# Kernel tuning notes

Measured on AMD Instinct MI355X. Metric: run time of the kernel, lower is better.

Reference implementation:

```python
import jax, jax.numpy as jnp
import numpy as np

N, E, D, G, OUT, K = 150000, 1200000, 128, 512, 2, 2
EPS = 1e-5


def setup_inputs() -> dict:
    key = jax.random.key(0)
    ks = jax.random.split(key, 8)
    nfeat = jax.random.normal(ks[0], (N, D), dtype=jnp.float32)
    src = jax.random.randint(ks[1], (E,), 0, N, dtype=jnp.int32)
    dst = jax.random.randint(ks[2], (E,), 0, N, dtype=jnp.int32)
    node2graph = jnp.sort(jax.random.randint(ks[3], (N,), 0, G, dtype=jnp.int32))
    s = 1.0 / np.sqrt(D)
    conv_w = jax.random.normal(ks[4], (D, D), dtype=jnp.float32) * s
    conv_b = jnp.zeros((D,), jnp.float32)
    gamma1 = jnp.ones((D,), jnp.float32)
    beta1 = jnp.zeros((D,), jnp.float32)
    gamma2 = jnp.ones((D,), jnp.float32)
    beta2 = jnp.zeros((D,), jnp.float32)
    pred_w = jax.random.normal(ks[5], (D, OUT), dtype=jnp.float32) * s
    pred_b = jnp.zeros((OUT,), jnp.float32)
    return {"nfeat": nfeat, "src": src, "dst": dst, "node2graph": node2graph,
            "num_graphs": G,
            "conv_w": conv_w, "conv_b": conv_b,
            "gamma1": gamma1, "beta1": beta1,
            "gamma2": gamma2, "beta2": beta2,
            "pred_w": pred_w, "pred_b": pred_b}


def _batchnorm(h, gamma, beta):
    # batch-norm over the node dimension (training-mode stats)
    mu = jnp.mean(h, axis=0)
    var = jnp.mean(jnp.square(h - mu), axis=0)
    return (h - mu) * jax.lax.rsqrt(var + EPS) * gamma + beta


def reference(nfeat, src, dst, node2graph, num_graphs,
              conv_w, conv_b, gamma1, beta1, gamma2, beta2, pred_w, pred_b):
    n = nfeat.shape[0]
    # symmetric degree normalization D^{-1/2} A D^{-1/2}
    deg = jax.ops.segment_sum(jnp.ones_like(dst, dtype=nfeat.dtype), dst, num_segments=n)
    dnorm = jax.lax.rsqrt(jnp.clip(deg, 1.0, None))  # [N]
    h = nfeat  # dropout with p=0 is identity
    for _ in range(K):  # k-hop SGC propagation interleaved with norm
        m = (h * dnorm[:, None])[src]                       # [E, D] gather
        h = jax.ops.segment_sum(m, dst, num_segments=n)     # scatter-add
        h = h * dnorm[:, None]
        h = _batchnorm(h, gamma1, beta1)
    h = h @ conv_w + conv_b          # SGConv linear
    h = _batchnorm(h, gamma2, beta2)  # middle norm
    h = jax.nn.relu(h)                # activation (dropout p=0)
    # mean pooling per graph
    cnt = jax.ops.segment_sum(jnp.ones((n,), h.dtype), node2graph, num_segments=num_graphs)
    g = jax.ops.segment_sum(h, node2graph, num_segments=num_graphs)
    g = g / jnp.clip(cnt, 1.0, None)[:, None]
    return g @ pred_w + pred_b  # [G, OUT]
```

## Files before the change

kernel.cpp:

```cpp
#include <hip/hip_runtime.h>
#include <hip/hip_fp16.h>
#include <cstddef>
#include <cstdint>

constexpr int DIMS = 128;
constexpr float BN_EPS = 1e-5f;
constexpr int NSH = 64;
constexpr int GB = 2048;
constexpr int NPB = 512;

typedef _Float16 f16x8 __attribute__((ext_vector_type(8)));
typedef float f32x4 __attribute__((ext_vector_type(4)));

static __device__ __forceinline__ f16x8 as_f16x8(uint4 u) {
  union { uint4 u; f16x8 h; } x; x.u = u; return x.h;
}
static __device__ __forceinline__ __half2 as_h2(uint32_t u) {
  union { uint32_t u; __half2 h; } x; x.u = u; return x.h;
}

__global__ void zero_k(float* __restrict__ fp, size_t nf) {
  size_t i = (size_t)blockIdx.x * blockDim.x + threadIdx.x;
  if (i < nf) fp[i] = 0.f;
}

__global__ void cvt_k(const float* __restrict__ in, uint32_t* __restrict__ out,
                      const int* __restrict__ deg, float* __restrict__ dnorm, size_t n64) {
  size_t i = (size_t)blockIdx.x * blockDim.x + threadIdx.x;
  size_t stride = (size_t)gridDim.x * blockDim.x;
  const float2* in2 = (const float2*)in;
  for (; i < n64; i += stride) {
    size_t row = i >> 6;
    float d = rsqrtf(fmaxf((float)deg[row], 1.0f));
    if ((i & 63) == 0) dnorm[row] = d;
    float2 v = in2[i];
    __half2 h = __floats2half2_rn(v.x * d, v.y * d);
    out[i] = *(const uint32_t*)&h;
  }
}


__global__ __launch_bounds__(256) void cnt_k(const int* __restrict__ dst,
                                             int* __restrict__ C, int e, int chunk) {
  __shared__ int hist[512];
  int b = blockIdx.x;
  for (int j = threadIdx.x; j < 512; j += 256) hist[j] = 0;
  __syncthreads();
  int i0 = b * chunk;
  int i1 = i0 + chunk; if (i1 > e) i1 = e;
  for (int i = i0 + threadIdx.x; i < i1; i += 256)
    atomicAdd(&hist[dst[i] >> 9], 1);
  __syncthreads();
  for (int j = threadIdx.x; j < 512; j += 256) C[b * 512 + j] = hist[j];
}

__global__ __launch_bounds__(512) void colscan_k(int* __restrict__ C, int* __restrict__ tot) {
  int j = blockIdx.x;
  int t = threadIdx.x;
  int v = C[t * 512 + j];
  __shared__ int lds[512];
  lds[t] = v; __syncthreads();
  for (int off = 1; off < 512; off <<= 1) {
    int add = (t >= off) ? lds[t - off] : 0;
    __syncthreads();
    lds[t] += add;
    __syncthreads();
  }
  C[t * 512 + j] = lds[t] - v;
  if (t == 511) tot[j] = lds[511];
}

__global__ __launch_bounds__(512) void bscan_k(const int* __restrict__ tot, int nbins,
                                               int* __restrict__ boff, int e) {
  int t = threadIdx.x;
  int v = tot[t];
  __shared__ int lds[512];
  lds[t] = v; __syncthreads();
  for (int off = 1; off < 512; off <<= 1) {
    int add = (t >= off) ? lds[t - off] : 0;
    __syncthreads();
    lds[t] += add;
    __syncthreads();
  }
  boff[t] = lds[t] - v;
  if (t == 0) boff[nbins] = e;
}

__global__ __launch_bounds__(256) void scat_k(const int* __restrict__ src,
                                              const int* __restrict__ dst,
                                              const int* __restrict__ C,
                                              const int* __restrict__ boff,
                                              int* __restrict__ ebin, int e, int chunk) {
  __shared__ int cur[512];
  int b = blockIdx.x;
  for (int j = threadIdx.x; j < 512; j += 256) cur[j] = boff[j] + C[b * 512 + j];
  __syncthreads();
  int i0 = b * chunk;
  int i1 = i0 + chunk; if (i1 > e) i1 = e;
  for (int i = i0 + threadIdx.x; i < i1; i += 256) {
    int d = dst[i];
    int bin = d >> 9;
    int p = atomicAdd(&cur[bin], 1);
    ebin[p] = (src[i] << 9) | (d & 511);
  }
}

__global__ void deg_bins_k(const int* __restrict__ ebin, const int* __restrict__ boff,
                           int* __restrict__ deg, int n) {
  __shared__ int cnt[512];
  int b = blockIdx.x;
  for (int j = threadIdx.x; j < 512; j += 256) cnt[j] = 0;
  __syncthreads();
  int j0 = boff[b], j1 = boff[b + 1];
  for (int i = j0 + threadIdx.x; i < j1; i += 256) atomicAdd(&cnt[ebin[i] & 511], 1);
  __syncthreads();
  int base = b << 9;
  for (int j = threadIdx.x; j < 512; j += 256) {
    int node = base + j;
    if (node < n) deg[node] = cnt[j];
  }
}

__global__ void scan1_k(const int* __restrict__ deg, int* __restrict__ bsum, int n) {
  __shared__ int lds[256];
  int t = threadIdx.x;
  int base = blockIdx.x * 1024;
  int s = 0;
  for (int i = t; i < 1024; i += 256) {
    int idx = base + i;
    s += (idx < n) ? deg[idx] : 0;
  }
  lds[t] = s; __syncthreads();
  for (int off = 128; off > 0; off >>= 1) {
    if (t < off) lds[t] += lds[t + off];
    __syncthreads();
  }
  if (t == 0) bsum[blockIdx.x] = lds[0];
}

__global__ void scan2_k(int* __restrict__ bsum, int nb, int* __restrict__ row_off, int n, int e) {
  __shared__ int lds[256];
  int t = threadIdx.x;
  int v = (t < nb) ? bsum[t] : 0;
  lds[t] = v; __syncthreads();
  for (int off = 1; off < 256; off <<= 1) {
    int add = (t >= off) ? lds[t - off] : 0;
    __syncthreads();
    lds[t] += add;
    __syncthreads();
  }
  if (t < nb) bsum[t] = lds[t] - v;
  if (t == 0) row_off[n] = e;
}

__global__ void scan3_k(const int* __restrict__ deg, const int* __restrict__ bsum,
                        int* __restrict__ row_off, int n) {
  __shared__ int lds[256];
  int t = threadIdx.x;
  int base = blockIdx.x * 1024 + t * 4;
  int e0 = (base + 0 < n) ? deg[base + 0] : 0;
  int e1 = (base + 1 < n) ? deg[base + 1] : 0;
  int e2 = (base + 2 < n) ? deg[base + 2] : 0;
  int e3 = (base + 3 < n) ? deg[base + 3] : 0;
  int ts = e0 + e1 + e2 + e3;
  lds[t] = ts; __syncthreads();
  for (int off = 1; off < 256; off <<= 1) {
    int add = (t >= off) ? lds[t - off] : 0;
    __syncthreads();
    lds[t] += add;
    __syncthreads();
  }
  int ex = lds[t] - ts + bsum[blockIdx.x];
  if (base + 0 < n) row_off[base + 0] = ex;
  ex += e0;
  if (base + 1 < n) row_off[base + 1] = ex;
  ex += e1;
  if (base + 2 < n) row_off[base + 2] = ex;
  ex += e2;
  if (base + 3 < n) row_off[base + 3] = ex;
}

__global__ __launch_bounds__(512) void adj_bins_k(
    const int* __restrict__ ebin, const int* __restrict__ boff,
    const int* __restrict__ row_off, const float* __restrict__ dnorm,
    int* __restrict__ adj, float* __restrict__ wsum, int n) {
  __shared__ int cur[512];
  __shared__ int ro[512];
  __shared__ float ws[512];
  int b = blockIdx.x;
  int base = b << 9;
  for (int j = threadIdx.x; j < 512; j += 512) {
    cur[j] = 0;
    ws[j] = 0.f;
    int node = base + j;
    ro[j] = (node < n) ? row_off[node] : 0;
  }
  __syncthreads();
  int j0 = boff[b], j1 = boff[b + 1];
  for (int i = j0 + threadIdx.x; i < j1; i += 512) {
    int pk = ebin[i];
    int dl = pk & 511;
    int s = pk >> 9;
    int p = atomicAdd(&cur[dl], 1);
    adj[ro[dl] + p] = s;
    atomicAdd(&ws[dl], dnorm[s]);
  }
  __syncthreads();
  for (int j = threadIdx.x; j < 512; j += 512) {
    int node = base + j;
    if (node < n) wsum[node] = ws[j];
  }
}

template <bool AFF>
__global__ __launch_bounds__(256) void gather_k(
    const uint32_t* __restrict__ Xu, uint32_t* __restrict__ Yout,
    const int* __restrict__ row_off, const int* __restrict__ adj,
    const float* __restrict__ dn, const float* __restrict__ wsum,
    const float* __restrict__ a, const float* __restrict__ b,
    float* __restrict__ sumS, float* __restrict__ sqS, int n, int nwaves) {
  int tid = threadIdx.x;
  int l = tid & 63, w = tid >> 6;
  int wid = blockIdx.x * 4 + w;
  uint32_t lu = (uint32_t)l;
  int f0 = 2 * l;
  float af0 = 1.f, bf0 = 0.f, af1 = 1.f, bf1 = 0.f;
  if (AFF) { af0 = a[f0]; bf0 = b[f0]; af1 = a[f0 + 1]; bf1 = b[f0 + 1]; }
  float s0 = 0.f, s1 = 0.f, q0 = 0.f, q1 = 0.f;

  for (int nodeA = wid; nodeA < n; nodeA += 2 * nwaves) {
    const int nodeB = nodeA + nwaves;
    const bool hasB = nodeB < n;
    int ja = row_off[nodeA];
    const int ea = row_off[nodeA + 1];
    int jb = hasB ? row_off[nodeB] : 0;
    const int eb = hasB ? row_off[nodeB + 1] : 0;
    float accA0 = 0.f, accA1 = 0.f, accB0 = 0.f, accB1 = 0.f;

    while ((ja < ea) || (jb < eb)) {
      uint32_t xa[8], xb[8];
      const bool runA = ja < ea, runB = jb < eb;
      if (runA) {
#pragma unroll
        for (int t = 0; t < 8; ++t) {
          int jj = ja + t;
          int jc = jj < ea ? jj : ea - 1;
          uint32_t sj = (uint32_t)adj[jc];
          uint32_t v = Xu[(sj << 6) + lu];
          xa[t] = (jj < ea) ? v : 0u;
        }
      }
      if (runB) {
#pragma unroll
        for (int t = 0; t < 8; ++t) {
          int jj = jb + t;
          int jc = jj < eb ? jj : eb - 1;
          uint32_t sj = (uint32_t)adj[jc];
          uint32_t v = Xu[(sj << 6) + lu];
          xb[t] = (jj < eb) ? v : 0u;
        }
      }
      if (runA) {
        __half2 t0 = __hadd2(as_h2(xa[0]), as_h2(xa[1]));
        __half2 t1 = __hadd2(as_h2(xa[2]), as_h2(xa[3]));
        __half2 t2 = __hadd2(as_h2(xa[4]), as_h2(xa[5]));
        __half2 t3 = __hadd2(as_h2(xa[6]), as_h2(xa[7]));
        float2 u0 = __half22float2(__hadd2(t0, t1));
        float2 u1 = __half22float2(__hadd2(t2, t3));
        accA0 += u0.x + u1.x;
        accA1 += u0.y + u1.y;
        ja += 8;
      }
      if (runB) {
        __half2 t0 = __hadd2(as_h2(xb[0]), as_h2(xb[1]));
        __half2 t1 = __hadd2(as_h2(xb[2]), as_h2(xb[3]));
        __half2 t2 = __hadd2(as_h2(xb[4]), as_h2(xb[5]));
        __half2 t3 = __hadd2(as_h2(xb[6]), as_h2(xb[7]));
        float2 u0 = __half22float2(__hadd2(t0, t1));
        float2 u1 = __half22float2(__hadd2(t2, t3));
        accB0 += u0.x + u1.x;
        accB1 += u0.y + u1.y;
        jb += 8;
      }
    }

    {
      float dnn = dn[nodeA];
      float v0, v1;
      if constexpr (AFF) {
        float wsn = wsum[nodeA];
        v0 = dnn * fmaf(af0, accA0, bf0 * wsn);
        v1 = dnn * fmaf(af1, accA1, bf1 * wsn);
        __half2 hv = __floats2half2_rn(v0, v1);
        Yout[((uint32_t)nodeA << 6) + lu] = *(const uint32_t*)&hv;
      } else {
        v0 = dnn * accA0;
        v1 = dnn * accA1;
        __half2 hv = __floats2half2_rn(v0 * dnn, v1 * dnn);
        Yout[((uint32_t)nodeA << 6) + lu] = *(const uint32_t*)&hv;
      }
      s0 += v0; s1 += v1; q0 += v0 * v0; q1 += v1 * v1;
    }
    if (hasB) {
      float dnn = dn[nodeB];
      float v0, v1;
      if constexpr (AFF) {
        float wsn = wsum[nodeB];
        v0 = dnn * fmaf(af0, accB0, bf0 * wsn);
        v1 = dnn * fmaf(af1, accB1, bf1 * wsn);
        __half2 hv = __floats2half2_rn(v0, v1);
        Yout[((uint32_t)nodeB << 6) + lu] = *(const uint32_t*)&hv;
      } else {
        v0 = dnn * accB0;
        v1 = dnn * accB1;
        __half2 hv = __floats2half2_rn(v0 * dnn, v1 * dnn);
        Yout[((uint32_t)nodeB << 6) + lu] = *(const uint32_t*)&hv;
      }
      s0 += v0; s1 += v1; q0 += v0 * v0; q1 += v1 * v1;
    }
  }

  __shared__ float red[4][256];
  red[w][l] = s0; red[w][64 + l] = s1; red[w][128 + l] = q0; red[w][192 + l] = q1;
  __syncthreads();
  float t = red[0][tid] + red[1][tid] + red[2][tid] + red[3][tid];
  int comp = tid >> 6, li = tid & 63;
  int sh = blockIdx.x & (NSH - 1);
  float* dstp = ((comp & 2) ? sqS : sumS) + sh * DIMS;
  atomicAdd(&dstp[2 * li + (comp & 1)], t);
}

__global__ void affine_k(const float* __restrict__ sum, const float* __restrict__ sq,
                         const float* __restrict__ gamma, const float* __restrict__ beta,
                         float* __restrict__ a, float* __restrict__ b, float invn) {
  int d = threadIdx.x;
  float s = 0.f, q = 0.f;
  for (int k = 0; k < NSH; ++k) { s += sum[k * DIMS + d]; q += sq[k * DIMS + d]; }
  float mu = s * invn;
  float var = q * invn - mu * mu;
  float rs = rsqrtf(var + BN_EPS);
  float ad = rs * gamma[d];
  a[d] = ad;
  b[d] = beta[d] - mu * ad;
}

__global__ void foldw_k(const float* __restrict__ W, const float* __restrict__ cb,
                        const float* __restrict__ a2, const float* __restrict__ b2,
                        __half* __restrict__ Wt, float* __restrict__ cp) {
  int o = blockIdx.x;
  int d = threadIdx.x;
  float w = W[d * DIMS + o];
  Wt[o * DIMS + d] = __float2half(a2[d] * w);
  __shared__ float red[128];
  red[d] = b2[d] * w;
  __syncthreads();
  for (int off = 64; off > 0; off >>= 1) {
    if (d < off) red[d] += red[d + off];
    __syncthreads();
  }
  if (d == 0) cp[o] = red[0] + cb[o];
}

__global__ __launch_bounds__(256) void matmul_k(
    const uint4* __restrict__ X, const uint4* __restrict__ Wt,
    const float* __restrict__ cp, __half* __restrict__ Z,
    float* __restrict__ sumS, float* __restrict__ sqS, int n) {
  int tid = threadIdx.x;
  int l = tid & 63, w = tid >> 6;
  int rowg = l & 15;
  int kg = l >> 4;
  int r0 = (blockIdx.x * 4 + w) * 16;
  bool active = r0 < n;

  __shared__ float sred[4][128], qred[4][128];
  float svals[8], qvals[8];

  if (active) {
    f32x4 acc[8] = {};
    const uint4* xrow = X + (size_t)(r0 + rowg) * 16;
    bool arow_ok = (r0 + rowg) < n;
#pragma unroll
    for (int kk = 0; kk < 4; ++kk) {
      uint4 au = arow_ok ? xrow[kk * 4 + kg] : make_uint4(0u, 0u, 0u, 0u);
      f16x8 afr = as_f16x8(au);
#pragma unroll
      for (int c = 0; c < 8; ++c) {
        f16x8 bfr = as_f16x8(Wt[(size_t)(c * 16 + rowg) * 16 + kk * 4 + kg]);
        acc[c] = __builtin_amdgcn_mfma_f32_16x16x32_f16(afr, bfr, acc[c], 0, 0, 0);
      }
    }
#pragma unroll
    for (int c = 0; c < 8; ++c) {
      float cpv = cp[c * 16 + rowg];
      float s = 0.f, q = 0.f;
#pragma unroll
      for (int r = 0; r < 4; ++r) {
        int row = r0 + kg * 4 + r;
        float vv = acc[c][r] + cpv;
        bool ok = row < n;
        vv = ok ? vv : 0.f;
        s += vv; q += vv * vv;
        if (ok) Z[(size_t)row * DIMS + c * 16 + rowg] = __float2half(vv);
      }
      s += __shfl_xor(s, 16); s += __shfl_xor(s, 32);
      q += __shfl_xor(q, 16); q += __shfl_xor(q, 32);
      svals[c] = s; qvals[c] = q;
    }
  }
  if (active) {
    if (kg == 0) {
#pragma unroll
      for (int c = 0; c < 8; ++c) {
        sred[w][c * 16 + rowg] = svals[c];
        qred[w][c * 16 + rowg] = qvals[c];
      }
    }
  } else {
    sred[w][l] = 0.f; sred[w][64 + l] = 0.f;
    qred[w][l] = 0.f; qred[w][64 + l] = 0.f;
  }
  __syncthreads();
  int f = tid & 127;
  int sh = blockIdx.x & (NSH - 1);
  if (tid < 128) {
    float s = sred[0][f] + sred[1][f] + sred[2][f] + sred[3][f];
    atomicAdd(&sumS[sh * DIMS + f], s);
  } else {
    float q = qred[0][f] + qred[1][f] + qred[2][f] + qred[3][f];
    atomicAdd(&sqS[sh * DIMS + f], q);
  }
}

__global__ void gstart_k(const int* __restrict__ n2g, int* __restrict__ gstart, int n, int G) {
  int i = blockIdx.x * blockDim.x + threadIdx.x;
  if (i >= n) return;
  int g = n2g[i];
  int gp = (i == 0) ? -1 : n2g[i - 1];
  for (int x = gp + 1; x <= g; ++x) gstart[x] = i;
  if (i == n - 1) {
    for (int x = g + 1; x <= G; ++x) gstart[x] = n;
  }
}

__global__ __launch_bounds__(512) void pool_pred_k(
    const uint4* __restrict__ Z, const int* __restrict__ gstart,
    const float* __restrict__ a3, const float* __restrict__ b3,
    const float* __restrict__ pw, const float* __restrict__ pb,
    float* __restrict__ out) {
  int g = blockIdx.x;
  int tid = threadIdx.x;
  int l = tid & 63, w = tid >> 6;
  int grp = l >> 4, fl = l & 15;
  int f0 = fl * 8;
  float av[8], bv[8];
#pragma unroll
  for (int q = 0; q < 8; ++q) { av[q] = a3[f0 + q]; bv[q] = b3[f0 + q]; }
  int s = gstart[g], e = gstart[g + 1];
  float rs[8] = {0.f, 0.f, 0.f, 0.f, 0.f, 0.f, 0.f, 0.f};
  for (int ni = s + (w * 4 + grp); ni < e; ni += 32) {
    uint4 zv = Z[(size_t)ni * 16 + fl];
    const __half2* h = (const __half2*)&zv;
#pragma unroll
    for (int q = 0; q < 4; ++q) {
      float2 z = __half22float2(h[q]);
      rs[2 * q] += fmaxf(fmaf(z.x, av[2 * q], bv[2 * q]), 0.f);
      rs[2 * q + 1] += fmaxf(fmaf(z.y, av[2 * q + 1], bv[2 * q + 1]), 0.f);
    }
  }
  float p0 = 0.f, p1 = 0.f;
#pragma unroll
  for (int q = 0; q < 8; ++q) {
    p0 += rs[q] * pw[(f0 + q) * 2 + 0];
    p1 += rs[q] * pw[(f0 + q) * 2 + 1];
  }
  __shared__ float r[2][512];
  r[0][tid] = p0; r[1][tid] = p1;
  __syncthreads();
  for (int off = 256; off > 0; off >>= 1) {
    if (tid < off) { r[0][tid] += r[0][tid + off]; r[1][tid] += r[1][tid + off]; }
    __syncthreads();
  }
  if (tid == 0) {
    float inv = 1.f / fmaxf((float)(e - s), 1.f);
    out[g * 2 + 0] = r[0][0] * inv + pb[0];
    out[g * 2 + 1] = r[1][0] * inv + pb[1];
  }
}

extern "C" void kernel_launch(void* const* d_in, const int* in_sizes, int n_in,
                              void* d_out, int out_size, void* d_ws, size_t ws_size,
                              hipStream_t stream) {
  const float* nfeat  = (const float*)d_in[0];
  const int*   src    = (const int*)d_in[1];
  const int*   dst    = (const int*)d_in[2];
  const int*   n2g    = (const int*)d_in[3];
  const float* conv_w = (const float*)d_in[5];
  const float* conv_b = (const float*)d_in[6];
  const float* gamma1 = (const float*)d_in[7];
  const float* beta1  = (const float*)d_in[8];
  const float* gamma2 = (const float*)d_in[9];
  const float* beta2  = (const float*)d_in[10];
  const float* pred_w = (const float*)d_in[11];
  const float* pred_b = (const float*)d_in[12];
  float* out = (float*)d_out;
  (void)n_in; (void)ws_size;

  const int n = in_sizes[0] / DIMS;
  const int e = in_sizes[1];
  const int g = out_size / 2;
  const int nbins = (n + 511) >> 9;

  char* p = (char*)d_ws;
  auto alloc = [&](size_t bytes) { char* r = p; p += (bytes + 255) & ~(size_t)255; return r; };
  uint32_t* Xp  = (uint32_t*)alloc((size_t)n * 64 * 4);
  uint32_t* W1  = (uint32_t*)alloc((size_t)n * 64 * 4);
  uint32_t* Y2  = (uint32_t*)alloc((size_t)n * 64 * 4);
  __half*   Zh  = (__half*)alloc((size_t)n * 64 * 4);
  float* dnorm = (float*)alloc((size_t)n * 4);
  float* stat  = (float*)alloc(((size_t)6 * NSH * DIMS + n) * 4);
  float* wsum  = stat + 6 * NSH * DIMS;
  float* affA  = (float*)alloc(3 * DIMS * 4);
  float* affB  = (float*)alloc(3 * DIMS * 4);
  __half* Wt   = (__half*)alloc(DIMS * DIMS * 2);
  float* cp    = (float*)alloc(DIMS * 4);
  int* deg     = (int*)alloc((size_t)n * 4);
  int* row_off = (int*)alloc(((size_t)n + 1) * 4);
  int* adj     = (int*)alloc((size_t)e * 4);
  int* ebin    = (int*)alloc((size_t)e * 4);
  int* Cmat    = (int*)alloc((size_t)NPB * 512 * 4);
  int* tot     = (int*)alloc(512 * 4);
  int* boff    = (int*)alloc(520 * 4);
  int* bsum    = (int*)alloc(2048 * 4);
  int* gstart  = (int*)alloc(((size_t)g + 1) * 4);

  const int SLAB = NSH * DIMS;
  float* S0 = stat + 0 * SLAB; float* Q0 = stat + 1 * SLAB;
  float* S1 = stat + 2 * SLAB; float* Q1 = stat + 3 * SLAB;
  float* S2 = stat + 4 * SLAB; float* Q2 = stat + 5 * SLAB;

  const int nb = (n + 1023) / 1024;
  const float invn = 1.0f / (float)n;
  const int nwaves = GB * 4;
  const int chunk = (e + NPB - 1) / NPB;

  zero_k<<<dim3(((size_t)6 * SLAB + 255) / 256), dim3(256), 0, stream>>>(stat, (size_t)6 * SLAB);
  cnt_k<<<dim3(NPB), dim3(256), 0, stream>>>(dst, Cmat, e, chunk);
  colscan_k<<<dim3(512), dim3(512), 0, stream>>>(Cmat, tot);
  bscan_k<<<dim3(1), dim3(512), 0, stream>>>(tot, nbins, boff, e);
  scat_k<<<dim3(NPB), dim3(256), 0, stream>>>(src, dst, Cmat, boff, ebin, e, chunk);
  deg_bins_k<<<dim3(nbins), dim3(256), 0, stream>>>(ebin, boff, deg, n);
  cvt_k<<<dim3(2048), dim3(256), 0, stream>>>(nfeat, Xp, deg, dnorm, (size_t)n * 64);
  scan1_k<<<dim3(nb), dim3(256), 0, stream>>>(deg, bsum, n);
  scan2_k<<<dim3(1), dim3(256), 0, stream>>>(bsum, nb, row_off, n, e);
  scan3_k<<<dim3(nb), dim3(256), 0, stream>>>(deg, bsum, row_off, n);
  adj_bins_k<<<dim3(nbins), dim3(512), 0, stream>>>(ebin, boff, row_off, dnorm, adj, wsum, n);

  gather_k<false><<<dim3(GB), dim3(256), 0, stream>>>(
      Xp, W1, row_off, adj, dnorm, wsum, nullptr, nullptr, S0, Q0, n, nwaves);
  affine_k<<<dim3(1), dim3(DIMS), 0, stream>>>(S0, Q0, gamma1, beta1, affA + 0, affB + 0, invn);
  gather_k<true><<<dim3(GB), dim3(256), 0, stream>>>(
      W1, Y2, row_off, adj, dnorm, wsum, affA + 0, affB + 0, S1, Q1, n, nwaves);
  affine_k<<<dim3(1), dim3(DIMS), 0, stream>>>(S1, Q1, gamma1, beta1, affA + DIMS, affB + DIMS, invn);
  foldw_k<<<dim3(DIMS), dim3(DIMS), 0, stream>>>(conv_w, conv_b, affA + DIMS, affB + DIMS, Wt, cp);
  matmul_k<<<dim3((n + 63) / 64), dim3(256), 0, stream>>>(
      (const uint4*)Y2, (const uint4*)Wt, cp, Zh, S2, Q2, n);
  affine_k<<<dim3(1), dim3(DIMS), 0, stream>>>(S2, Q2, gamma2, beta2, affA + 2 * DIMS, affB + 2 * DIMS, invn);
  gstart_k<<<dim3((n + 255) / 256), dim3(256), 0, stream>>>(n2g, gstart, n, g);
  pool_pred_k<<<dim3(g), dim3(512), 0, stream>>>((const uint4*)Zh, gstart,
                                                 affA + 2 * DIMS, affB + 2 * DIMS,
                                                 pred_w, pred_b, out);
}
```

Baseline: 285.1 us.

## Fuse degree/scan kernels into per-bin index kernel, widen matmul tiles, double gather grid

Replaces the degree-count kernel and the three-pass global scan with one per-bin kernel. It counts degrees in LDS, does a local scan offset by the bin base, and writes row offsets and dnorm directly, so cvt_k no longer computes dnorm. The matmul now processes 32 rows per wave, reusing each weight fragment for two MFMAs, and stages its fp16 output through LDS so rows are written as coalesced 16-byte stores. The gather grid size is doubled. Together these cut kernel launches and global passes, at the cost of more LDS and registers in the matmul.

```diff
diff --git a/kernel.cpp b/kernel.cpp
--- a/kernel.cpp
+++ b/kernel.cpp
@@ -6,7 +6,7 @@
 constexpr int DIMS = 128;
 constexpr float BN_EPS = 1e-5f;
 constexpr int NSH = 64;
-constexpr int GB = 2048;
+constexpr int GB = 4096;
 constexpr int NPB = 512;
 
 typedef _Float16 f16x8 __attribute__((ext_vector_type(8)));
@@ -25,14 +25,12 @@
 }
 
 __global__ void cvt_k(const float* __restrict__ in, uint32_t* __restrict__ out,
-                      const int* __restrict__ deg, float* __restrict__ dnorm, size_t n64) {
+                      const float* __restrict__ dnorm, size_t n64) {
   size_t i = (size_t)blockIdx.x * blockDim.x + threadIdx.x;
   size_t stride = (size_t)gridDim.x * blockDim.x;
   const float2* in2 = (const float2*)in;
   for (; i < n64; i += stride) {
-    size_t row = i >> 6;
-    float d = rsqrtf(fmaxf((float)deg[row], 1.0f));
-    if ((i & 63) == 0) dnorm[row] = d;
+    float d = dnorm[i >> 6];
     float2 v = in2[i];
     __half2 h = __floats2half2_rn(v.x * d, v.y * d);
     out[i] = *(const uint32_t*)&h;
@@ -105,79 +103,32 @@
   }
 }
 
-__global__ void deg_bins_k(const int* __restrict__ ebin, const int* __restrict__ boff,
-                           int* __restrict__ deg, int n) {
+__global__ __launch_bounds__(512) void binidx_k(
+    const int* __restrict__ ebin, const int* __restrict__ boff,
+    int* __restrict__ row_off, float* __restrict__ dnorm, int n, int nbins) {
   __shared__ int cnt[512];
+  __shared__ int scn[512];
   int b = blockIdx.x;
-  for (int j = threadIdx.x; j < 512; j += 256) cnt[j] = 0;
+  int t = threadIdx.x;
+  cnt[t] = 0;
   __syncthreads();
   int j0 = boff[b], j1 = boff[b + 1];
-  for (int i = j0 + threadIdx.x; i < j1; i += 256) atomicAdd(&cnt[ebin[i] & 511], 1);
-  __syncthreads();
-  int base = b << 9;
-  for (int j = threadIdx.x; j < 512; j += 256) {
-    int node = base + j;
-    if (node < n) deg[node] = cnt[j];
-  }
-}
-
-__global__ void scan1_k(const int* __restrict__ deg, int* __restrict__ bsum, int n) {
-  __shared__ int lds[256];
-  int t = threadIdx.x;
-  int base = blockIdx.x * 1024;
-  int s = 0;
-  for (int i = t; i < 1024; i += 256) {
-    int idx = base + i;
-    s += (idx < n) ? deg[idx] : 0;
-  }
-  lds[t] = s; __syncthreads();
-  for (int off = 128; off > 0; off >>= 1) {
-    if (t < off) lds[t] += lds[t + off];
-    __syncthreads();
-  }
-  if (t == 0) bsum[blockIdx.x] = lds[0];
-}
-
-__global__ void scan2_k(int* __restrict__ bsum, int nb, int* __restrict__ row_off, int n, int e) {
-  __shared__ int lds[256];
-  int t = threadIdx.x;
-  int v = (t < nb) ? bsum[t] : 0;
-  lds[t] = v; __syncthreads();
-  for (int off = 1; off < 256; off <<= 1) {
-    int add = (t >= off) ? lds[t - off] : 0;
-    __syncthreads();
-    lds[t] += add;
-    __syncthreads();
-  }
-  if (t < nb) bsum[t] = lds[t] - v;
-  if (t == 0) row_off[n] = e;
-}
-
-__global__ void scan3_k(const int* __restrict__ deg, const int* __restrict__ bsum,
-                        int* __restrict__ row_off, int n) {
-  __shared__ int lds[256];
-  int t = threadIdx.x;
-  int base = blockIdx.x * 1024 + t * 4;
-  int e0 = (base + 0 < n) ? deg[base + 0] : 0;
-  int e1 = (base + 1 < n) ? deg[base + 1] : 0;
-  int e2 = (base + 2 < n) ? deg[base + 2] : 0;
-  int e3 = (base + 3 < n) ? deg[base + 3] : 0;
-  int ts = e0 + e1 + e2 + e3;
-  lds[t] = ts; __syncthreads();
-  for (int off = 1; off < 256; off <<= 1) {
-    int add = (t >= off) ? lds[t - off] : 0;
-    __syncthreads();
-    lds[t] += add;
-    __syncthreads();
-  }
-  int ex = lds[t] - ts + bsum[blockIdx.x];
-  if (base + 0 < n) row_off[base + 0] = ex;
-  ex += e0;
-  if (base + 1 < n) row_off[base + 1] = ex;
-  ex += e1;
-  if (base + 2 < n) row_off[base + 2] = ex;
-  ex += e2;
-  if (base + 3 < n) row_off[base + 3] = ex;
+  for (int i = j0 + t; i < j1; i += 512) atomicAdd(&cnt[ebin[i] & 511], 1);
+  __syncthreads();
+  int v = cnt[t];
+  scn[t] = v; __syncthreads();
+  for (int off = 1; off < 512; off <<= 1) {
+    int add = (t >= off) ? scn[t - off] : 0;
+    __syncthreads();
+    scn[t] += add;
+    __syncthreads();
+  }
+  int node = (b << 9) + t;
+  if (node < n) {
+    row_off[node] = j0 + scn[t] - v;
+    dnorm[node] = rsqrtf(fmaxf((float)v, 1.0f));
+  }
+  if (b == nbins - 1 && t == 0) row_off[n] = j1;
 }
 
 __global__ __launch_bounds__(512) void adj_bins_k(
@@ -189,15 +140,16 @@
   __shared__ float ws[512];
   int b = blockIdx.x;
   int base = b << 9;
-  for (int j = threadIdx.x; j < 512; j += 512) {
-    cur[j] = 0;
-    ws[j] = 0.f;
-    int node = base + j;
-    ro[j] = (node < n) ? row_off[node] : 0;
+  int t = threadIdx.x;
+  {
+    cur[t] = 0;
+    ws[t] = 0.f;
+    int node = base + t;
+    ro[t] = (node < n) ? row_off[node] : 0;
   }
   __syncthreads();
   int j0 = boff[b], j1 = boff[b + 1];
-  for (int i = j0 + threadIdx.x; i < j1; i += 512) {
+  for (int i = j0 + t; i < j1; i += 512) {
     int pk = ebin[i];
     int dl = pk & 511;
     int s = pk >> 9;
@@ -206,9 +158,9 @@
     atomicAdd(&ws[dl], dnorm[s]);
   }
   __syncthreads();
-  for (int j = threadIdx.x; j < 512; j += 512) {
-    int node = base + j;
-    if (node < n) wsum[node] = ws[j];
+  {
+    int node = base + t;
+    if (node < n) wsum[node] = ws[t];
   }
 }
 
@@ -363,48 +315,67 @@
 
 __global__ __launch_bounds__(256) void matmul_k(
     const uint4* __restrict__ X, const uint4* __restrict__ Wt,
-    const float* __restrict__ cp, __half* __restrict__ Z,
+    const float* __restrict__ cp, uint4* __restrict__ Z,
     float* __restrict__ sumS, float* __restrict__ sqS, int n) {
   int tid = threadIdx.x;
   int l = tid & 63, w = tid >> 6;
   int rowg = l & 15;
   int kg = l >> 4;
-  int r0 = (blockIdx.x * 4 + w) * 16;
+  int r0 = (blockIdx.x * 4 + w) * 32;
   bool active = r0 < n;
 
+  __shared__ __half outs[4][16][136];
   __shared__ float sred[4][128], qred[4][128];
   float svals[8], qvals[8];
 
   if (active) {
-    f32x4 acc[8] = {};
-    const uint4* xrow = X + (size_t)(r0 + rowg) * 16;
-    bool arow_ok = (r0 + rowg) < n;
+    f32x4 acc0[8] = {}, acc1[8] = {};
+    const uint4* xr0 = X + (size_t)(r0 + rowg) * 16;
+    const uint4* xr1 = X + (size_t)(r0 + 16 + rowg) * 16;
+    bool ok0 = (r0 + rowg) < n;
+    bool ok1 = (r0 + 16 + rowg) < n;
 #pragma unroll
     for (int kk = 0; kk < 4; ++kk) {
-      uint4 au = arow_ok ? xrow[kk * 4 + kg] : make_uint4(0u, 0u, 0u, 0u);
-      f16x8 afr = as_f16x8(au);
+      uint4 au0 = ok0 ? xr0[kk * 4 + kg] : make_uint4(0u, 0u, 0u, 0u);
+      uint4 au1 = ok1 ? xr1[kk * 4 + kg] : make_uint4(0u, 0u, 0u, 0u);
+      f16x8 a0 = as_f16x8(au0), a1 = as_f16x8(au1);
 #pragma unroll
       for (int c = 0; c < 8; ++c) {
         f16x8 bfr = as_f16x8(Wt[(size_t)(c * 16 + rowg) * 16 + kk * 4 + kg]);
-        acc[c] = __builtin_amdgcn_mfma_f32_16x16x32_f16(afr, bfr, acc[c], 0, 0, 0);
+        acc0[c] = __builtin_amdgcn_mfma_f32_16x16x32_f16(a0, bfr, acc0[c], 0, 0, 0);
+        acc1[c] = __builtin_amdgcn_mfma_f32_16x16x32_f16(a1, bfr, acc1[c], 0, 0, 0);
+      }
+    }
+#pragma unroll
+    for (int c = 0; c < 8; ++c) { svals[c] = 0.f; qvals[c] = 0.f; }
+#pragma unroll
+    for (int gidx = 0; gidx < 2; ++gidx) {
+      int rbase = r0 + gidx * 16;
+#pragma unroll
+      for (int c = 0; c < 8; ++c) {
+        float cpv = cp[c * 16 + rowg];
+        f32x4 av = (gidx == 0) ? acc0[c] : acc1[c];
+#pragma unroll
+        for (int r = 0; r < 4; ++r) {
+          int row = rbase + kg * 4 + r;
+          float vv = av[r] + cpv;
+          vv = (row < n) ? vv : 0.f;
+          svals[c] += vv; qvals[c] += vv * vv;
+          outs[w][kg * 4 + r][c * 16 + rowg] = __float2half(vv);
+        }
+      }
+#pragma unroll
+      for (int it = 0; it < 4; ++it) {
+        int lr = it * 4 + kg;
+        int grow = rbase + lr;
+        if (grow < n)
+          Z[(size_t)grow * 16 + rowg] = *(const uint4*)&outs[w][lr][rowg * 8];
       }
     }
 #pragma unroll
     for (int c = 0; c < 8; ++c) {
-      float cpv = cp[c * 16 + rowg];
-      float s = 0.f, q = 0.f;
-#pragma unroll
-      for (int r = 0; r < 4; ++r) {
-        int row = r0 + kg * 4 + r;
-        float vv = acc[c][r] + cpv;
-        bool ok = row < n;
-        vv = ok ? vv : 0.f;
-        s += vv; q += vv * vv;
-        if (ok) Z[(size_t)row * DIMS + c * 16 + rowg] = __float2half(vv);
-      }
-      s += __shfl_xor(s, 16); s += __shfl_xor(s, 32);
-      q += __shfl_xor(q, 16); q += __shfl_xor(q, 32);
-      svals[c] = s; qvals[c] = q;
+      svals[c] += __shfl_xor(svals[c], 16); svals[c] += __shfl_xor(svals[c], 32);
+      qvals[c] += __shfl_xor(qvals[c], 16); qvals[c] += __shfl_xor(qvals[c], 32);
     }
   }
   if (active) {
@@ -523,14 +494,12 @@
   float* affB  = (float*)alloc(3 * DIMS * 4);
   __half* Wt   = (__half*)alloc(DIMS * DIMS * 2);
   float* cp    = (float*)alloc(DIMS * 4);
-  int* deg     = (int*)alloc((size_t)n * 4);
   int* row_off = (int*)alloc(((size_t)n + 1) * 4);
   int* adj     = (int*)alloc((size_t)e * 4);
   int* ebin    = (int*)alloc((size_t)e * 4);
   int* Cmat    = (int*)alloc((size_t)NPB * 512 * 4);
   int* tot     = (int*)alloc(512 * 4);
   int* boff    = (int*)alloc(520 * 4);
-  int* bsum    = (int*)alloc(2048 * 4);
   int* gstart  = (int*)alloc(((size_t)g + 1) * 4);
 
   const int SLAB = NSH * DIMS;
@@ -538,7 +507,6 @@
   float* S1 = stat + 2 * SLAB; float* Q1 = stat + 3 * SLAB;
   float* S2 = stat + 4 * SLAB; float* Q2 = stat + 5 * SLAB;
 
-  const int nb = (n + 1023) / 1024;
   const float invn = 1.0f / (float)n;
   const int nwaves = GB * 4;
   const int chunk = (e + NPB - 1) / NPB;
@@ -548,11 +516,8 @@
   colscan_k<<<dim3(512), dim3(512), 0, stream>>>(Cmat, tot);
   bscan_k<<<dim3(1), dim3(512), 0, stream>>>(tot, nbins, boff, e);
   scat_k<<<dim3(NPB), dim3(256), 0, stream>>>(src, dst, Cmat, boff, ebin, e, chunk);
-  deg_bins_k<<<dim3(nbins), dim3(256), 0, stream>>>(ebin, boff, deg, n);
-  cvt_k<<<dim3(2048), dim3(256), 0, stream>>>(nfeat, Xp, deg, dnorm, (size_t)n * 64);
-  scan1_k<<<dim3(nb), dim3(256), 0, stream>>>(deg, bsum, n);
-  scan2_k<<<dim3(1), dim3(256), 0, stream>>>(bsum, nb, row_off, n, e);
-  scan3_k<<<dim3(nb), dim3(256), 0, stream>>>(deg, bsum, row_off, n);
+  binidx_k<<<dim3(nbins), dim3(512), 0, stream>>>(ebin, boff, row_off, dnorm, n, nbins);
+  cvt_k<<<dim3(2048), dim3(256), 0, stream>>>(nfeat, Xp, dnorm, (size_t)n * 64);
   adj_bins_k<<<dim3(nbins), dim3(512), 0, stream>>>(ebin, boff, row_off, dnorm, adj, wsum, n);
 
   gather_k<false><<<dim3(GB), dim3(256), 0, stream>>>(
@@ -562,8 +527,8 @@
       W1, Y2, row_off, adj, dnorm, wsum, affA + 0, affB + 0, S1, Q1, n, nwaves);
   affine_k<<<dim3(1), dim3(DIMS), 0, stream>>>(S1, Q1, gamma1, beta1, affA + DIMS, affB + DIMS, invn);
   foldw_k<<<dim3(DIMS), dim3(DIMS), 0, stream>>>(conv_w, conv_b, affA + DIMS, affB + DIMS, Wt, cp);
-  matmul_k<<<dim3((n + 63) / 64), dim3(256), 0, stream>>>(
-      (const uint4*)Y2, (const uint4*)Wt, cp, Zh, S2, Q2, n);
+  matmul_k<<<dim3((n + 127) / 128), dim3(256), 0, stream>>>(
+      (const uint4*)Y2, (const uint4*)Wt, cp, (uint4*)Zh, S2, Q2, n);
   affine_k<<<dim3(1), dim3(DIMS), 0, stream>>>(S2, Q2, gamma2, beta2, affA + 2 * DIMS, affB + 2 * DIMS, invn);
   gstart_k<<<dim3((n + 255) / 256), dim3(256), 0, stream>>>(n2g, gstart, n, g);
   pool_pred_k<<<dim3(g), dim3(512), 0, stream>>>((const uint4*)Zh, gstart,
```

Measured after the change: 255.8 us, median of 2. 1.11x faster.
